# Kernel tuning notes

Measured on AMD Instinct MI355X. Metric: run time of the kernel, lower is better.

The kernel has to match this reference:

```python
import jax, jax.numpy as jnp
import numpy as np

B, S, D, H = 2, 2048, 1024, 16
DH = D // H


def setup_inputs() -> dict:
    key = jax.random.key(0)
    ks = jax.random.split(key, 6)
    std = 1.0 / np.sqrt(D)
    return {
        "x": jax.random.normal(ks[0], (B, S, D), dtype=jnp.float32),
        "Wq": jax.random.normal(ks[1], (D, D), dtype=jnp.float32) * std,
        "bq": jnp.zeros((D,), dtype=jnp.float32),
        "Wk": jax.random.normal(ks[2], (D, D), dtype=jnp.float32) * std,
        "bk": jnp.zeros((D,), dtype=jnp.float32),
        "Wv": jax.random.normal(ks[3], (D, D), dtype=jnp.float32) * std,
        "bv": jnp.zeros((D,), dtype=jnp.float32),
        "Wo": jax.random.normal(ks[4], (D, D), dtype=jnp.float32) * std,
        "bo": jnp.zeros((D,), dtype=jnp.float32),
        "slopes": jax.random.uniform(ks[5], (H,), dtype=jnp.float32) * 0.1 + 0.05,
    }


def _attention(x, Wq, bq, Wk, bk, Wv, bv, Wo, bo, slopes):
    # projections: [B,S,D] -> [B,H,S,Dh]
    def split_heads(t):
        return t.reshape(B, S, H, DH).transpose(0, 2, 1, 3)

    q = split_heads(x @ Wq + bq)
    k = split_heads(x @ Wk + bk)
    v = split_heads(x @ Wv + bv)

    scale = jnp.sqrt(jnp.asarray(DH, dtype=x.dtype))
    logits = jnp.einsum("bhsd,bhtd->bhst", q, k) / scale  # [B,H,S,S]

    pos = jnp.arange(S, dtype=x.dtype)
    dist = jnp.abs(pos[:, None] - pos[None, :])            # [S,S]
    bias = -jax.nn.softplus(slopes)[:, None, None] * dist  # [H,S,S]
    logits = logits + bias[None]

    attn = jax.nn.softmax(logits, axis=-1)
    out = jnp.einsum("bhst,bhtd->bhsd", attn, v)           # [B,H,S,Dh]
    out = out.transpose(0, 2, 1, 3).reshape(B, S, D)
    return out @ Wo + bo


def reference(x, Wq, bq, Wk, bk, Wv, bv, Wo, bo, slopes):
    return _attention(x, Wq, bq, Wk, bk, Wv, bv, Wo, bo, slopes)
```

## Files before the change

kernel.cpp:

```cpp
#include <hip/hip_runtime.h>

typedef unsigned short u16;
typedef unsigned int u32;
typedef short bf16x8 __attribute__((ext_vector_type(8)));
typedef float f32x4 __attribute__((ext_vector_type(4)));

#define S_LEN 2048
#define DMODEL 1024
#define NHEAD 16
#define DHEAD 64
#define MROWS 4096

typedef __attribute__((address_space(1))) const void gas_t;
typedef __attribute__((address_space(3))) void las_t;

__device__ __forceinline__ float bf2f(u16 u) {
    union { u32 i; float f; } c; c.i = ((u32)u) << 16; return c.f;
}
__device__ __forceinline__ u16 f2bf(float f) {
    union { float f; u32 i; } c; c.f = f;
    u32 u = c.i;
    u32 r = (u + 0x7fffu + ((u >> 16) & 1u)) >> 16;
    return (u16)r;
}

__global__ __launch_bounds__(256) void cvt_x(
    const float* __restrict__ x, u16* __restrict__ xb)
{
    const size_t i = ((size_t)blockIdx.x * 256 + threadIdx.x) * 8;
    float v[8];
    __builtin_memcpy(v, &x[i], 32);
    u16 o[8];
#pragma unroll
    for (int j = 0; j < 8; ++j) o[j] = f2bf(v[j]);
    __builtin_memcpy(&xb[i], o, 16);
}

__global__ __launch_bounds__(256) void cvt_w(
    const float* __restrict__ W0, const float* __restrict__ W1,
    const float* __restrict__ W2, const float* __restrict__ W3,
    u16* __restrict__ WT)
{
    __shared__ u16 T[64][65];
    const int which = blockIdx.z;
    const float* W = which == 0 ? W0 : which == 1 ? W1 : which == 2 ? W2 : W3;
    const int n0 = blockIdx.x << 6, k0 = blockIdx.y << 6;
    const int r = threadIdx.x >> 2, c0 = (threadIdx.x & 3) << 4;

    float v[16];
    __builtin_memcpy(v, &W[(size_t)(k0 + r) * DMODEL + n0 + c0], 64);
    u16 o[16];
#pragma unroll
    for (int j = 0; j < 16; ++j) o[j] = f2bf(v[j]);
    __builtin_memcpy(&T[r][c0], o, 32);
    __syncthreads();

    u16 t[16];
#pragma unroll
    for (int j = 0; j < 16; ++j) t[j] = T[c0 + j][r];
    __builtin_memcpy(&WT[((size_t)(which * DMODEL + n0 + r)) * DMODEL + k0 + c0], t, 32);
}

template<bool QKV>
__global__ __launch_bounds__(256) void gemm128(
    const u16* __restrict__ A, const u16* __restrict__ WT,
    const float* __restrict__ b0, const float* __restrict__ b1,
    const float* __restrict__ b2,
    u16* __restrict__ o0, u16* __restrict__ o1, u16* __restrict__ o2,
    float* __restrict__ outf)
{
    __shared__ __align__(16) u16 As[128 * 32];
    __shared__ __align__(16) u16 Bs[128 * 32];

    const int tid  = threadIdx.x;
    const int w    = tid >> 6;
    const int lane = tid & 63;
    const int l15  = lane & 15;
    const int quad = lane >> 4;
    const int wm   = w & 1, wn = w >> 1;
    const int m0   = blockIdx.y << 7;
    const int n0   = blockIdx.x << 7;

    const int lr = lane >> 2;
    const int lc = (lane & 3) << 3;
    const u16* Ag0 = A  + (size_t)(m0 + (w << 5) + lr) * DMODEL + lc;
    const u16* Ag1 = Ag0 + 16 * DMODEL;
    const u16* Bg0 = WT + (size_t)(n0 + (w << 5) + lr) * DMODEL + lc;
    const u16* Bg1 = Bg0 + 16 * DMODEL;
    u16* Al0 = &As[((w << 5) + 0) << 5];
    u16* Al1 = &As[((w << 5) + 16) << 5];
    u16* Bl0 = &Bs[((w << 5) + 0) << 5];
    u16* Bl1 = &Bs[((w << 5) + 16) << 5];

    f32x4 acc[4][4];
#pragma unroll
    for (int i = 0; i < 4; ++i)
#pragma unroll
        for (int j = 0; j < 4; ++j) acc[i][j] = (f32x4){0.f, 0.f, 0.f, 0.f};

    for (int k0 = 0; k0 < DMODEL; k0 += 32) {
        __syncthreads();
        __builtin_amdgcn_global_load_lds((gas_t*)(Ag0 + k0), (las_t*)Al0, 16, 0, 0);
        __builtin_amdgcn_global_load_lds((gas_t*)(Ag1 + k0), (las_t*)Al1, 16, 0, 0);
        __builtin_amdgcn_global_load_lds((gas_t*)(Bg0 + k0), (las_t*)Bl0, 16, 0, 0);
        __builtin_amdgcn_global_load_lds((gas_t*)(Bg1 + k0), (las_t*)Bl1, 16, 0, 0);
        __syncthreads();

        bf16x8 af[4], bfr[4];
#pragma unroll
        for (int mt = 0; mt < 4; ++mt)
            __builtin_memcpy(&af[mt], &As[(((wm << 6) + (mt << 4) + l15) << 5) + (quad << 3)], 16);
#pragma unroll
        for (int nt = 0; nt < 4; ++nt)
            __builtin_memcpy(&bfr[nt], &Bs[(((wn << 6) + (nt << 4) + l15) << 5) + (quad << 3)], 16);
#pragma unroll
        for (int mt = 0; mt < 4; ++mt)
#pragma unroll
            for (int nt = 0; nt < 4; ++nt)
                acc[mt][nt] = __builtin_amdgcn_mfma_f32_16x16x32_bf16(af[mt], bfr[nt], acc[mt][nt], 0, 0, 0);
    }

#pragma unroll
    for (int nt = 0; nt < 4; ++nt) {
        const int col = n0 + (wn << 6) + (nt << 4) + l15;
        if (QKV) {
            const int proj = col >> 10;
            const int c    = col & (DMODEL - 1);
            const float* bb = proj == 0 ? b0 : proj == 1 ? b1 : b2;
            u16* dst        = proj == 0 ? o0 : proj == 1 ? o1 : o2;
            const float bvv = bb[c];
            const int h = c >> 6, dh = c & (DHEAD - 1);
            const bool tr = (proj == 2);
#pragma unroll
            for (int mt = 0; mt < 4; ++mt)
#pragma unroll
                for (int r = 0; r < 4; ++r) {
                    const int row = m0 + (wm << 6) + (mt << 4) + (quad << 2) + r;
                    const int b = row >> 11, s = row & (S_LEN - 1);
                    const size_t idx = tr
                        ? ((size_t)((b << 4) + h) * DHEAD + dh) * S_LEN + s
                        : ((size_t)((b << 4) + h) * S_LEN + s) * DHEAD + dh;
                    dst[idx] = f2bf(acc[mt][nt][r] + bvv);
                }
        } else {
            const float bvv = b0[col];
#pragma unroll
            for (int mt = 0; mt < 4; ++mt)
#pragma unroll
                for (int r = 0; r < 4; ++r) {
                    const int row = m0 + (wm << 6) + (mt << 4) + (quad << 2) + r;
                    outf[(size_t)row * DMODEL + col] = acc[mt][nt][r] + bvv;
                }
        }
    }
}

__global__ __launch_bounds__(256) void attn_mfma(
    const u16* __restrict__ q, const u16* __restrict__ k,
    const u16* __restrict__ vt, const float* __restrict__ slopes,
    u16* __restrict__ ctx)
{
    __shared__ __align__(16) u16 Ks[64 * 64];
    __shared__ __align__(16) u16 Vs[64 * 64];
    __shared__ __align__(16) u16 Ps[64][72];

    const int tid  = threadIdx.x;
    const int w    = tid >> 6;
    const int lane = tid & 63;
    const int l15  = lane & 15;
    const int quad = lane >> 4;
    const int bh   = blockIdx.y;
    const int h    = bh & (NHEAD - 1);
    const int q0   = blockIdx.x << 6;

    const float LOG2E = 1.4426950408889634f;
    const float sp  = logf(1.f + __expf(slopes[h]));
    const float sp2 = sp * LOG2E;
    const float c1  = 0.125f * LOG2E;

    const int srow  = (w << 4) + (lane >> 3);
    const int schnk = (lane & 7) ^ ((lane >> 3) & 7);
    const u16* kg = k  + (size_t)bh * S_LEN * DHEAD + (size_t)srow * DHEAD + (schnk << 3);
    const u16* vg = vt + (size_t)bh * DHEAD * S_LEN + (size_t)srow * S_LEN + (schnk << 3);
    u16* kl = &Ks[(w << 4) << 6];
    u16* vl = &Vs[(w << 4) << 6];

    bf16x8 qf[2];
    {
        const u16* qrow = q + ((size_t)bh * S_LEN + q0 + (w << 4) + l15) * DHEAD + (quad << 3);
        __builtin_memcpy(&qf[0], qrow, 16);
        __builtin_memcpy(&qf[1], qrow + 32, 16);
    }

    f32x4 accO[4];
#pragma unroll
    for (int i = 0; i < 4; ++i) accO[i] = (f32x4){0.f, 0.f, 0.f, 0.f};
    float lp[4] = {0.f, 0.f, 0.f, 0.f};

    float fq[4];
#pragma unroll
    for (int r = 0; r < 4; ++r) fq[r] = (float)(q0 + (w << 4) + (quad << 2) + r);

    const int tq   = q0 >> 6;
    const int t_lo = tq - 2 < 0 ? 0 : tq - 2;
    const int t_hi = tq + 2 > (S_LEN >> 6) - 1 ? (S_LEN >> 6) - 1 : tq + 2;

    for (int tt = t_lo; tt <= t_hi; ++tt) {
        const int kt0 = tt << 6;
        __syncthreads();
        __builtin_amdgcn_global_load_lds((gas_t*)(kg + (size_t)kt0 * DHEAD),
                                         (las_t*)kl, 16, 0, 0);
        __builtin_amdgcn_global_load_lds((gas_t*)(kg + (size_t)(kt0 + 8) * DHEAD),
                                         (las_t*)(kl + 8 * 64), 16, 0, 0);
        __builtin_amdgcn_global_load_lds((gas_t*)(vg + kt0),
                                         (las_t*)vl, 16, 0, 0);
        __builtin_amdgcn_global_load_lds((gas_t*)(vg + kt0 + 8 * S_LEN),
                                         (las_t*)(vl + 8 * 64), 16, 0, 0);
        __syncthreads();

        f32x4 accS[4];
#pragma unroll
        for (int i = 0; i < 4; ++i) accS[i] = (f32x4){0.f, 0.f, 0.f, 0.f};
#pragma unroll
        for (int kc = 0; kc < 2; ++kc) {
#pragma unroll
            for (int nt = 0; nt < 4; ++nt) {
                bf16x8 kf;
                const int koff = (((nt << 4) + l15) << 6)
                               + ((((kc << 2) + quad) ^ (l15 & 7)) << 3);
                __builtin_memcpy(&kf, &Ks[koff], 16);
                accS[nt] = __builtin_amdgcn_mfma_f32_16x16x32_bf16(qf[kc], kf, accS[nt], 0, 0, 0);
            }
        }

#pragma unroll
        for (int nt = 0; nt < 4; ++nt) {
            const float fk = (float)(kt0 + (nt << 4) + l15);
#pragma unroll
            for (int r = 0; r < 4; ++r) {
                const float d = fabsf(fq[r] - fk);
                const float p = exp2f(fmaf(accS[nt][r], c1, -sp2 * d));
                lp[r] += p;
                const int row = (w << 4) + (quad << 2) + r;
                const int col = ((nt << 4) + l15) ^ (quad << 4);
                Ps[row][col] = f2bf(p);
            }
        }

#pragma unroll
        for (int kc = 0; kc < 2; ++kc) {
            bf16x8 pf;
            const int pcol = ((kc << 5) + (quad << 3)) ^ (((l15 >> 2) & 3) << 4);
            __builtin_memcpy(&pf, &Ps[(w << 4) + l15][pcol], 16);
#pragma unroll
            for (int nt = 0; nt < 4; ++nt) {
                bf16x8 vf;
                const int voff = (((nt << 4) + l15) << 6)
                               + ((((kc << 2) + quad) ^ (l15 & 7)) << 3);
                __builtin_memcpy(&vf, &Vs[voff], 16);
                accO[nt] = __builtin_amdgcn_mfma_f32_16x16x32_bf16(pf, vf, accO[nt], 0, 0, 0);
            }
        }
    }

#pragma unroll
    for (int r = 0; r < 4; ++r) {
        float t = lp[r];
        t += __shfl_xor(t, 1, 64);
        t += __shfl_xor(t, 2, 64);
        t += __shfl_xor(t, 4, 64);
        t += __shfl_xor(t, 8, 64);
        lp[r] = 1.f / t;
    }
    const int b = bh >> 4;
#pragma unroll
    for (int r = 0; r < 4; ++r) {
        const int s = q0 + (w << 4) + (quad << 2) + r;
        u16* crow = ctx + ((size_t)(b * S_LEN + s)) * DMODEL + h * DHEAD;
#pragma unroll
        for (int nt = 0; nt < 4; ++nt)
            crow[(nt << 4) + l15] = f2bf(accO[nt][r] * lp[r]);
    }
}

extern "C" void kernel_launch(void* const* d_in, const int* in_sizes, int n_in,
                              void* d_out, int out_size, void* d_ws, size_t ws_size,
                              hipStream_t stream) {
    const float* x      = (const float*)d_in[0];
    const float* Wq     = (const float*)d_in[1];
    const float* bq     = (const float*)d_in[2];
    const float* Wk     = (const float*)d_in[3];
    const float* bk     = (const float*)d_in[4];
    const float* Wv     = (const float*)d_in[5];
    const float* bv     = (const float*)d_in[6];
    const float* Wo     = (const float*)d_in[7];
    const float* bo     = (const float*)d_in[8];
    const float* slopes = (const float*)d_in[9];

    u16* ws = (u16*)d_ws;
    const size_t NEL = (size_t)MROWS * DMODEL;
    u16* xb  = ws;
    u16* ctx = ws;
    u16* WT  = ws + NEL;
    u16* kb  = ws + 2 * NEL;
    u16* qb  = (u16*)d_out;
    u16* vb;
    if (ws_size >= 4 * NEL * sizeof(u16)) vb = ws + 3 * NEL;
    else                                  vb = (u16*)d_out + NEL;

    dim3 blk(256);
    cvt_x<<<MROWS * DMODEL / (8 * 256), blk, 0, stream>>>(x, xb);
    cvt_w<<<dim3(16, 16, 4), blk, 0, stream>>>(Wq, Wk, Wv, Wo, WT);

    gemm128<true><<<dim3(3 * DMODEL / 128, MROWS / 128), blk, 0, stream>>>(
        xb, WT, bq, bk, bv, qb, kb, vb, nullptr);

    attn_mfma<<<dim3(S_LEN / 64, 2 * NHEAD), blk, 0, stream>>>(qb, kb, vb, slopes, ctx);

    gemm128<false><<<dim3(DMODEL / 128, MROWS / 128), blk, 0, stream>>>(
        ctx, WT + 3 * (size_t)DMODEL * DMODEL, bo, nullptr, nullptr,
        nullptr, nullptr, nullptr, (float*)d_out);
}
```

Before: 197.7 us.

## Double GEMM K-tile with XOR-swizzled LDS and merge conversion kernels

The GEMM K-step grows from 32 to 64, halving the number of barrier pairs per tile, and the LDS layout gets an XOR swizzle on 16-byte chunks to avoid bank conflicts on fragment reads. The x and weight conversion kernels are fused into one launch using an extra grid z-slice, removing one kernel launch. Doubled LDS per block (32 KB) may reduce occupancy.

```diff
diff --git a/kernel.cpp b/kernel.cpp
--- a/kernel.cpp
+++ b/kernel.cpp
@@ -24,26 +24,29 @@
     return (u16)r;
 }
 
-__global__ __launch_bounds__(256) void cvt_x(
-    const float* __restrict__ x, u16* __restrict__ xb)
-{
-    const size_t i = ((size_t)blockIdx.x * 256 + threadIdx.x) * 8;
-    float v[8];
-    __builtin_memcpy(v, &x[i], 32);
-    u16 o[8];
-#pragma unroll
-    for (int j = 0; j < 8; ++j) o[j] = f2bf(v[j]);
-    __builtin_memcpy(&xb[i], o, 16);
-}
-
-__global__ __launch_bounds__(256) void cvt_w(
+__global__ __launch_bounds__(256) void cvt_all(
+    const float* __restrict__ x, u16* __restrict__ xb,
     const float* __restrict__ W0, const float* __restrict__ W1,
     const float* __restrict__ W2, const float* __restrict__ W3,
     u16* __restrict__ WT)
 {
+    const int z = blockIdx.z;
+    if (z == 4) {
+        const size_t base = ((size_t)(blockIdx.y * 16 + blockIdx.x)) * 16384;
+#pragma unroll
+        for (int j = 0; j < 8; ++j) {
+            const size_t i = base + (size_t)j * 2048 + threadIdx.x * 8;
+            float v[8];
+            __builtin_memcpy(v, &x[i], 32);
+            u16 o[8];
+#pragma unroll
+            for (int t = 0; t < 8; ++t) o[t] = f2bf(v[t]);
+            __builtin_memcpy(&xb[i], o, 16);
+        }
+        return;
+    }
     __shared__ u16 T[64][65];
-    const int which = blockIdx.z;
-    const float* W = which == 0 ? W0 : which == 1 ? W1 : which == 2 ? W2 : W3;
+    const float* W = z == 0 ? W0 : z == 1 ? W1 : z == 2 ? W2 : W3;
     const int n0 = blockIdx.x << 6, k0 = blockIdx.y << 6;
     const int r = threadIdx.x >> 2, c0 = (threadIdx.x & 3) << 4;
 
@@ -58,7 +61,7 @@
     u16 t[16];
 #pragma unroll
     for (int j = 0; j < 16; ++j) t[j] = T[c0 + j][r];
-    __builtin_memcpy(&WT[((size_t)(which * DMODEL + n0 + r)) * DMODEL + k0 + c0], t, 32);
+    __builtin_memcpy(&WT[((size_t)(z * DMODEL + n0 + r)) * DMODEL + k0 + c0], t, 32);
 }
 
 template<bool QKV>
@@ -69,8 +72,8 @@
     u16* __restrict__ o0, u16* __restrict__ o1, u16* __restrict__ o2,
     float* __restrict__ outf)
 {
-    __shared__ __align__(16) u16 As[128 * 32];
-    __shared__ __align__(16) u16 Bs[128 * 32];
+    __shared__ __align__(16) u16 As[128 * 64];
+    __shared__ __align__(16) u16 Bs[128 * 64];
 
     const int tid  = threadIdx.x;
     const int w    = tid >> 6;
@@ -81,16 +84,12 @@
     const int m0   = blockIdx.y << 7;
     const int n0   = blockIdx.x << 7;
 
-    const int lr = lane >> 2;
-    const int lc = (lane & 3) << 3;
-    const u16* Ag0 = A  + (size_t)(m0 + (w << 5) + lr) * DMODEL + lc;
-    const u16* Ag1 = Ag0 + 16 * DMODEL;
-    const u16* Bg0 = WT + (size_t)(n0 + (w << 5) + lr) * DMODEL + lc;
-    const u16* Bg1 = Bg0 + 16 * DMODEL;
-    u16* Al0 = &As[((w << 5) + 0) << 5];
-    u16* Al1 = &As[((w << 5) + 16) << 5];
-    u16* Bl0 = &Bs[((w << 5) + 0) << 5];
-    u16* Bl1 = &Bs[((w << 5) + 16) << 5];
+    const int rg = lane >> 3;
+    const int gc = ((lane & 7) ^ rg) << 3;
+    const u16* Ag = A  + (size_t)(m0 + (w << 5) + rg) * DMODEL + gc;
+    const u16* Bg = WT + (size_t)(n0 + (w << 5) + rg) * DMODEL + gc;
+    u16* Al = &As[((w << 5) + 0) << 6];
+    u16* Bl = &Bs[((w << 5) + 0) << 6];
 
     f32x4 acc[4][4];
 #pragma unroll
@@ -98,26 +97,38 @@
 #pragma unroll
         for (int j = 0; j < 4; ++j) acc[i][j] = (f32x4){0.f, 0.f, 0.f, 0.f};
 
-    for (int k0 = 0; k0 < DMODEL; k0 += 32) {
+    for (int k0 = 0; k0 < DMODEL; k0 += 64) {
         __syncthreads();
-        __builtin_amdgcn_global_load_lds((gas_t*)(Ag0 + k0), (las_t*)Al0, 16, 0, 0);
-        __builtin_amdgcn_global_load_lds((gas_t*)(Ag1 + k0), (las_t*)Al1, 16, 0, 0);
-        __builtin_amdgcn_global_load_lds((gas_t*)(Bg0 + k0), (las_t*)Bl0, 16, 0, 0);
-        __builtin_amdgcn_global_load_lds((gas_t*)(Bg1 + k0), (las_t*)Bl1, 16, 0, 0);
+#pragma unroll
+        for (int i = 0; i < 4; ++i) {
+            __builtin_amdgcn_global_load_lds((gas_t*)(Ag + k0 + (size_t)(i << 3) * DMODEL),
+                                             (las_t*)(Al + ((i << 3) << 6)), 16, 0, 0);
+            __builtin_amdgcn_global_load_lds((gas_t*)(Bg + k0 + (size_t)(i << 3) * DMODEL),
+                                             (las_t*)(Bl + ((i << 3) << 6)), 16, 0, 0);
+        }
         __syncthreads();
 
-        bf16x8 af[4], bfr[4];
-#pragma unroll
-        for (int mt = 0; mt < 4; ++mt)
-            __builtin_memcpy(&af[mt], &As[(((wm << 6) + (mt << 4) + l15) << 5) + (quad << 3)], 16);
-#pragma unroll
-        for (int nt = 0; nt < 4; ++nt)
-            __builtin_memcpy(&bfr[nt], &Bs[(((wn << 6) + (nt << 4) + l15) << 5) + (quad << 3)], 16);
-#pragma unroll
-        for (int mt = 0; mt < 4; ++mt)
-#pragma unroll
-            for (int nt = 0; nt < 4; ++nt)
-                acc[mt][nt] = __builtin_amdgcn_mfma_f32_16x16x32_bf16(af[mt], bfr[nt], acc[mt][nt], 0, 0, 0);
+#pragma unroll
+        for (int kc = 0; kc < 2; ++kc) {
+            bf16x8 af[4], bfr[4];
+#pragma unroll
+            for (int mt = 0; mt < 4; ++mt) {
+                const int row = (wm << 6) + (mt << 4) + l15;
+                const int ch  = (((kc << 2) + quad) ^ (l15 & 7)) << 3;
+                __builtin_memcpy(&af[mt], &As[(row << 6) + ch], 16);
+            }
+#pragma unroll
+            for (int nt = 0; nt < 4; ++nt) {
+                const int row = (wn << 6) + (nt << 4) + l15;
+                const int ch  = (((kc << 2) + quad) ^ (l15 & 7)) << 3;
+                __builtin_memcpy(&bfr[nt], &Bs[(row << 6) + ch], 16);
+            }
+#pragma unroll
+            for (int mt = 0; mt < 4; ++mt)
+#pragma unroll
+                for (int nt = 0; nt < 4; ++nt)
+                    acc[mt][nt] = __builtin_amdgcn_mfma_f32_16x16x32_bf16(af[mt], bfr[nt], acc[mt][nt], 0, 0, 0);
+        }
     }
 
 #pragma unroll
@@ -309,8 +320,7 @@
     else                                  vb = (u16*)d_out + NEL;
 
     dim3 blk(256);
-    cvt_x<<<MROWS * DMODEL / (8 * 256), blk, 0, stream>>>(x, xb);
-    cvt_w<<<dim3(16, 16, 4), blk, 0, stream>>>(Wq, Wk, Wv, Wo, WT);
+    cvt_all<<<dim3(16, 16, 5), blk, 0, stream>>>(x, xb, Wq, Wk, Wv, Wo, WT);
 
     gemm128<true><<<dim3(3 * DMODEL / 128, MROWS / 128), blk, 0, stream>>>(
         xb, WT, bq, bk, bv, qb, kb, vb, nullptr);
```

After: 183.5 us. 7.2% less time.
